# Kernel optimization log

Measured on AMD Instinct MI355X. Metric: run time of the kernel, lower is better.

Reference implementation:

```python
import jax, jax.numpy as jnp
import numpy as np

N_NODES = 100000
N_EDGES = 3200000
OUT_FEATURES = 16


def setup_inputs() -> dict:
    key = jax.random.key(0)
    k1, k2 = jax.random.split(key)
    edge = jax.random.randint(k1, (2, N_EDGES), 0, N_NODES, dtype=jnp.int64 if jax.config.jax_enable_x64 else jnp.int32)
    edge_w = jax.random.normal(k2, (N_EDGES, OUT_FEATURES), dtype=jnp.float32)
    return {
        "edge": edge,
        "edge_w": edge_w,
        "N": N_NODES,
        "E": N_EDGES,
        "out_features": OUT_FEATURES,
    }


def reference(edge, edge_w, N, E, out_features):
    # torch.sparse.sum over dim=1 of a [N, N, F] COO tensor == segment-sum of
    # edge_w grouped by the source index edge[0], producing dense [N, F].
    src = edge[0]  # [E]
    out = jax.ops.segment_sum(edge_w, src, num_segments=N)  # [N, F]
    return out
```

## Files before the change

kernel.cpp:

```cpp
#include <hip/hip_runtime.h>
#include <hip/hip_cooperative_groups.h>
#include <math.h>

namespace cg = cooperative_groups;


#define F 16
#define NPB 1024
#define NPB_SHIFT 10
#define MAXB 128
#define SCALE 256.0f
#define INV_SCALE (1.0f / 256.0f)

#define NBIN 256
#define BINT 512
#define NSPLIT 8
#define SLICES (NBIN / NSPLIT)
#define ACCT 512

#define FB 512
#define FT 512
#define NBIN2 512
#define NSPLIT2 8
#define SLICES2 (NBIN2 / NSPLIT2)

__device__ __forceinline__ unsigned long long qpack(float4 v) {
    long long q0 = (long long)__float2int_rn(v.x * SCALE);
    long long q1 = (long long)__float2int_rn(v.y * SCALE);
    long long q2 = (long long)__float2int_rn(v.z * SCALE);
    long long q3 = (long long)__float2int_rn(v.w * SCALE);
    return (unsigned long long)((q3 << 48) + (q2 << 32) + (q1 << 16) + q0);
}

__global__ __launch_bounds__(FT, 4) void spmm_fused(
    const int* __restrict__ src,
    const float* __restrict__ w,
    unsigned int* __restrict__ idbuf,
    unsigned int* __restrict__ cnt,
    unsigned long long* __restrict__ pbuf,
    float* __restrict__ out,
    int E, int B, int capb, int per_block, int N)
{
    __shared__ unsigned long long acc[NPB * 4];
    __shared__ unsigned int pos[MAXB];
    __shared__ unsigned int ksh[SLICES2];

    cg::grid_group grid = cg::this_grid();
    const int tid = threadIdx.x;
    const int bid = blockIdx.x;
    const int n4  = N * 4;
    unsigned long long* spill = pbuf + (size_t)NSPLIT2 * (size_t)n4;

    for (int i = tid; i < B; i += FT) pos[i] = 0;
    __syncthreads();

    const int lo = bid * per_block;
    const int hi = min(E, lo + per_block);
    for (int e = lo + tid * 2; e < hi; e += FT * 2) {
        int sa, sb = -1;
        if (e + 1 < hi) { int2 s2 = *(const int2*)(src + e); sa = s2.x; sb = s2.y; }
        else            { sa = src[e]; }
        {
            const int bk = sa >> NPB_SHIFT;
            const unsigned int off = (unsigned int)(sa & (NPB - 1));
            const unsigned int r = atomicAdd(&pos[bk], 1u);
            if (r < (unsigned int)capb) {
                idbuf[((size_t)bid * B + bk) * capb + r] = (off << 22) | (unsigned int)e;
            } else {
                const float4* wr = (const float4*)(w + (size_t)e * F);
                #pragma unroll
                for (int qq = 0; qq < 4; ++qq)
                    atomicAdd(&spill[(size_t)sa * 4 + qq], qpack(wr[qq]));
            }
        }
        if (sb >= 0) {
            const int e1 = e + 1;
            const int bk = sb >> NPB_SHIFT;
            const unsigned int off = (unsigned int)(sb & (NPB - 1));
            const unsigned int r = atomicAdd(&pos[bk], 1u);
            if (r < (unsigned int)capb) {
                idbuf[((size_t)bid * B + bk) * capb + r] = (off << 22) | (unsigned int)e1;
            } else {
                const float4* wr = (const float4*)(w + (size_t)e1 * F);
                #pragma unroll
                for (int qq = 0; qq < 4; ++qq)
                    atomicAdd(&spill[(size_t)sb * 4 + qq], qpack(wr[qq]));
            }
        }
    }
    __syncthreads();
    for (int i = tid; i < B; i += FT)
        cnt[bid * B + i] = min(pos[i], (unsigned int)capb);

    __threadfence();
    grid.sync();

    const int q    = tid & 3;
    const int ei   = tid >> 2;
    const int half = ei >> 6;
    const int e64  = ei & 63;

    for (int t = bid; t < B * NSPLIT2; t += FB) {
        const int b  = t >> 3;
        const int sp = t & 7;

        for (int i = tid; i < NPB * 4; i += FT) acc[i] = 0ULL;
        if (tid < SLICES2) ksh[tid] = cnt[(sp * SLICES2 + tid) * B + b];
        __syncthreads();

        for (int sl = 0; sl < SLICES2; sl += 16) {
            unsigned int ent[8];
            #pragma unroll
            for (int j = 0; j < 8; ++j) {
                const int s = sl + 2 * j + half;
                ent[j] = idbuf[((size_t)(sp * SLICES2 + s) * B + b) * capb + e64];
            }
            float4 vv[8];
            #pragma unroll
            for (int j = 0; j < 8; ++j) {
                unsigned int e = ent[j] & 0x3FFFFFu;
                e = min(e, (unsigned int)(E - 1));
                vv[j] = *(const float4*)(w + (size_t)e * F + q * 4);
            }
            #pragma unroll
            for (int j = 0; j < 8; ++j) {
                const int s = sl + 2 * j + half;
                if ((unsigned int)e64 < ksh[s]) {
                    const unsigned int off = ent[j] >> 22;
                    atomicAdd(&acc[off * 4 + q], qpack(vv[j]));
                }
            }
        }
        for (int s = half; s < SLICES2; s += 2) {
            const unsigned int k = ksh[s];
            for (unsigned int i = 64 + e64; i < k; i += 64) {
                const unsigned int entry =
                    idbuf[((size_t)(sp * SLICES2 + s) * B + b) * capb + i];
                const unsigned int off = entry >> 22;
                const unsigned int e   = entry & 0x3FFFFFu;
                const float4 v = *(const float4*)(w + (size_t)e * F + q * 4);
                atomicAdd(&acc[off * 4 + q], qpack(v));
            }
        }
        __syncthreads();

        const int nbase = b << NPB_SHIFT;
        const int lim = min(NPB, N - nbase);
        unsigned long long* dst = pbuf + (size_t)sp * n4 + (size_t)nbase * 4;
        for (int i = tid; i < lim * 4; i += FT) dst[i] = acc[i];
        __syncthreads();
    }

    __threadfence();
    grid.sync();

    for (int idx = bid * FT + tid; idx < n4; idx += FB * FT) {
        unsigned long long a = 0;
        #pragma unroll
        for (int s = 0; s < NSPLIT2 + 1; ++s) a += pbuf[(size_t)s * n4 + idx];
        long long tt = (long long)a;
        const int s0 = (int)(short)(tt & 0xffff);  tt = (tt - s0) >> 16;
        const int s1 = (int)(short)(tt & 0xffff);  tt = (tt - s1) >> 16;
        const int s2 = (int)(short)(tt & 0xffff);  tt = (tt - s2) >> 16;
        const int s3 = (int)(short)(tt & 0xffff);
        float4 o;
        o.x = (float)s0 * INV_SCALE;
        o.y = (float)s1 * INV_SCALE;
        o.z = (float)s2 * INV_SCALE;
        o.w = (float)s3 * INV_SCALE;
        ((float4*)out)[idx] = o;
    }
}

__global__ __launch_bounds__(BINT) void spmm_bin_id(
    const int* __restrict__ src,
    const float* __restrict__ w,
    unsigned int* __restrict__ idbuf,
    unsigned int* __restrict__ cnt,
    unsigned long long* __restrict__ spill,
    int E, int B, int capb, int per_block)
{
    __shared__ unsigned int pos[MAXB];
    const int tid = threadIdx.x;
    for (int i = tid; i < B; i += BINT) pos[i] = 0;
    __syncthreads();

    const int lo = blockIdx.x * per_block;
    const int hi = min(E, lo + per_block);

    for (int e = lo + tid; e < hi; e += BINT) {
        const int s = src[e];
        const int bk = s >> NPB_SHIFT;
        const unsigned int off = (unsigned int)(s & (NPB - 1));
        const unsigned int r = atomicAdd(&pos[bk], 1u);
        if (r < (unsigned int)capb) {
            idbuf[((size_t)blockIdx.x * B + bk) * capb + r] =
                (off << 22) | (unsigned int)e;
        } else {
            const float4* wr = (const float4*)(w + (size_t)e * F);
            #pragma unroll
            for (int q = 0; q < 4; ++q)
                atomicAdd(&spill[(size_t)s * 4 + q], qpack(wr[q]));
        }
    }
    __syncthreads();
    for (int i = tid; i < B; i += BINT)
        cnt[blockIdx.x * B + i] = min(pos[i], (unsigned int)capb);
}

__global__ __launch_bounds__(ACCT) void spmm_acc_g(
    const float* __restrict__ w,
    const unsigned int* __restrict__ idbuf,
    const unsigned int* __restrict__ cnt,
    unsigned long long* __restrict__ pbuf,
    int B, int capb, int N)
{
    __shared__ unsigned long long acc[NPB * 4];
    const int tid = threadIdx.x;
    const int b  = blockIdx.x >> 3;
    const int sp = blockIdx.x & 7;

    for (int i = tid; i < NPB * 4; i += ACCT) acc[i] = 0ULL;
    __syncthreads();

    const int q  = tid & 3;
    const int ei = tid >> 2;

    for (int sl = 0; sl < SLICES; ++sl) {
        const int blk = sp * SLICES + sl;
        const unsigned int k = cnt[blk * B + b];
        const unsigned int* base = idbuf + ((size_t)blk * B + b) * capb;
        for (unsigned int i = ei; i < k; i += ACCT / 4) {
            const unsigned int entry = base[i];
            const unsigned int off = entry >> 22;
            const unsigned int e   = entry & 0x3FFFFFu;
            const float4 v = *(const float4*)(w + (size_t)e * F + q * 4);
            atomicAdd(&acc[off * 4 + q], qpack(v));
        }
    }
    __syncthreads();

    const int nbase = b << NPB_SHIFT;
    const int lim = min(NPB, N - nbase);
    unsigned long long* dst = pbuf + (size_t)sp * ((size_t)N * 4) + (size_t)nbase * 4;
    for (int i = tid; i < lim * 4; i += ACCT) dst[i] = acc[i];
}

__global__ __launch_bounds__(256) void spmm_decode9(
    const unsigned long long* __restrict__ pbuf,
    float* __restrict__ out, int n4)
{
    const int idx = blockIdx.x * 256 + threadIdx.x;
    if (idx >= n4) return;
    unsigned long long a = 0;
    #pragma unroll
    for (int s = 0; s < NSPLIT + 1; ++s) a += pbuf[(size_t)s * n4 + idx];

    long long t = (long long)a;
    const int s0 = (int)(short)(t & 0xffff);  t = (t - s0) >> 16;
    const int s1 = (int)(short)(t & 0xffff);  t = (t - s1) >> 16;
    const int s2 = (int)(short)(t & 0xffff);  t = (t - s2) >> 16;
    const int s3 = (int)(short)(t & 0xffff);

    float4 o;
    o.x = (float)s0 * INV_SCALE;
    o.y = (float)s1 * INV_SCALE;
    o.z = (float)s2 * INV_SCALE;
    o.w = (float)s3 * INV_SCALE;
    ((float4*)out)[idx] = o;
}

__global__ __launch_bounds__(256) void spmm_scatter_gs(
    const int* __restrict__ src,
    const float* __restrict__ w,
    unsigned long long* __restrict__ ws,
    int total)
{
    const int stride = gridDim.x * blockDim.x;
    for (int idx = blockIdx.x * blockDim.x + threadIdx.x; idx < total; idx += stride) {
        const int e = idx >> 2, lane = idx & 3;
        const float4 v = ((const float4*)w)[idx];
        atomicAdd(&ws[src[e] * 4 + lane], qpack(v));
    }
}

__global__ __launch_bounds__(256) void spmm_decode1(
    const unsigned long long* __restrict__ ws,
    float* __restrict__ out, int n4)
{
    const int idx = blockIdx.x * 256 + threadIdx.x;
    if (idx >= n4) return;
    long long t = (long long)ws[idx];
    const int s0 = (int)(short)(t & 0xffff);  t = (t - s0) >> 16;
    const int s1 = (int)(short)(t & 0xffff);  t = (t - s1) >> 16;
    const int s2 = (int)(short)(t & 0xffff);  t = (t - s2) >> 16;
    const int s3 = (int)(short)(t & 0xffff);
    float4 o;
    o.x = (float)s0 * INV_SCALE;
    o.y = (float)s1 * INV_SCALE;
    o.z = (float)s2 * INV_SCALE;
    o.w = (float)s3 * INV_SCALE;
    ((float4*)out)[idx] = o;
}

extern "C" void kernel_launch(void* const* d_in, const int* in_sizes, int n_in,
                              void* d_out, int out_size, void* d_ws, size_t ws_size,
                              hipStream_t stream) {
    const int* edge = (const int*)d_in[0];
    const float* ew = (const float*)d_in[1];
    const int E = in_sizes[0] / 2;
    const int N = out_size / F;
    const int n4 = N * 4;
    float* out = (float*)d_out;

    const int B = (N + NPB - 1) >> NPB_SHIFT;

    static int coop_state = -1;
    if (coop_state < 0) {
        int maxb = 0, cus = 0;
        hipDeviceProp_t prop;
        int dev = 0;
        hipError_t e1 = hipGetDevice(&dev);
        hipError_t e2 = hipGetDeviceProperties(&prop, dev);
        if (e2 == hipSuccess) cus = prop.multiProcessorCount;
        hipError_t e3 = hipOccupancyMaxActiveBlocksPerMultiprocessor(
            &maxb, spmm_fused, FT, 0);
        coop_state = (e1 == hipSuccess && e3 == hipSuccess &&
                      (long)maxb * (long)cus >= FB) ? 1 : 0;
    }

    const double mean2 = (double)E / ((double)NBIN2 * (double)B);
    int capb2 = (int)(mean2 + 8.0 * sqrt(mean2 > 1.0 ? mean2 : 1.0) + 16.0);
    capb2 = (capb2 + 15) & ~15;
    const size_t idbuf2_b = (size_t)NBIN2 * B * capb2 * 4;
    size_t off_cnt2  = (idbuf2_b + 255) & ~(size_t)255;
    const size_t cnt2_b = (size_t)NBIN2 * B * 4;
    size_t off_pbuf2 = (off_cnt2 + cnt2_b + 255) & ~(size_t)255;
    const size_t pbuf2_b = (size_t)(NSPLIT2 + 1) * n4 * 8;
    const size_t need2 = off_pbuf2 + pbuf2_b;

    const double mean = (double)E / ((double)NBIN * (double)B);
    int capb = (int)(mean + 8.0 * sqrt(mean > 1.0 ? mean : 1.0) + 16.0);
    capb = (capb + 15) & ~15;
    const size_t idbuf_b = (size_t)NBIN * B * capb * 4;
    size_t off_cnt  = (idbuf_b + 255) & ~(size_t)255;
    const size_t cnt_b = (size_t)NBIN * B * 4;
    size_t off_pbuf = (off_cnt + cnt_b + 255) & ~(size_t)255;
    const size_t pbuf_b = (size_t)(NSPLIT + 1) * n4 * 8;
    const size_t need = off_pbuf + pbuf_b;

    const int block = 256;
    const bool shape_ok = (B <= MAXB) && (E > 0) && (E < (1 << 22));

    if (shape_ok && coop_state == 1 && need2 <= ws_size) {
        unsigned int* idbuf = (unsigned int*)d_ws;
        unsigned int* cnt   = (unsigned int*)((char*)d_ws + off_cnt2);
        unsigned long long* pbuf = (unsigned long long*)((char*)d_ws + off_pbuf2);
        unsigned long long* spill = pbuf + (size_t)NSPLIT2 * n4;

        hipMemsetAsync(spill, 0, (size_t)n4 * 8, stream);

        int per_block2 = (E + FB - 1) / FB;
        per_block2 = (per_block2 + 1) & ~1;

        int E_ = E, B_ = B, N_ = N, cap_ = capb2, pb_ = per_block2;
        void* kargs[] = { (void*)&edge, (void*)&ew, (void*)&idbuf, (void*)&cnt,
                          (void*)&pbuf, (void*)&out,
                          (void*)&E_, (void*)&B_, (void*)&cap_, (void*)&pb_, (void*)&N_ };
        hipError_t lr = hipLaunchCooperativeKernel(
            spmm_fused, dim3(FB), dim3(FT), kargs, 0, stream);
        if (lr == hipSuccess) return;
        coop_state = 0;
    }

    if (shape_ok && need <= ws_size) {
        unsigned int* idbuf = (unsigned int*)d_ws;
        unsigned int* cnt   = (unsigned int*)((char*)d_ws + off_cnt);
        unsigned long long* pbuf  = (unsigned long long*)((char*)d_ws + off_pbuf);
        unsigned long long* spill = pbuf + (size_t)NSPLIT * n4;

        hipMemsetAsync(spill, 0, (size_t)n4 * 8, stream);

        const int per_block = (E + NBIN - 1) / NBIN;
        spmm_bin_id<<<NBIN, BINT, 0, stream>>>(edge, ew, idbuf, cnt, spill,
                                               E, B, capb, per_block);
        spmm_acc_g<<<B * NSPLIT, ACCT, 0, stream>>>(ew, idbuf, cnt, pbuf,
                                                    B, capb, N);
        spmm_decode9<<<(n4 + block - 1) / block, block, 0, stream>>>(pbuf, out, n4);
    } else {
        unsigned long long* ws = (unsigned long long*)d_ws;
        hipMemsetAsync(ws, 0, (size_t)n4 * 8, stream);
        spmm_scatter_gs<<<2048, block, 0, stream>>>(edge, ew, ws, E * 4);
        spmm_decode1<<<(n4 + block - 1) / block, block, 0, stream>>>(ws, out, n4);
    }
}
```

Measured before the change: 355.6 us.

## Double cooperative grid and bin count, remap slice-gather threads, fit capacity to workspace

Doubles the cooperative grid to 1024 blocks and the per-block source bins to 1024, raising the launch-bounds occupancy hint to 8 blocks. The gather phase is reorganised so 16 lanes per slice walk up to 64 entries with a count guard. This replaces the unconditional clamped loads of the old code. Entries past 64 are now handled by a single thread per slice in a serial loop. Bucket capacity uses a tighter margin and is capped to the available workspace, with a minimum-capacity check before the fused path is chosen. More blocks and bins aim to spread the binning and accumulation work across more of the device, at the cost of smaller per-bin lists, a serial overflow tail and a larger count array.

```diff
diff --git a/kernel.cpp b/kernel.cpp
--- a/kernel.cpp
+++ b/kernel.cpp
@@ -18,9 +18,9 @@
 #define SLICES (NBIN / NSPLIT)
 #define ACCT 512
 
-#define FB 512
+#define FB 1024
 #define FT 512
-#define NBIN2 512
+#define NBIN2 1024
 #define NSPLIT2 8
 #define SLICES2 (NBIN2 / NSPLIT2)
 
@@ -32,7 +32,7 @@
     return (unsigned long long)((q3 << 48) + (q2 << 32) + (q1 << 16) + q0);
 }
 
-__global__ __launch_bounds__(FT, 4) void spmm_fused(
+__global__ __launch_bounds__(FT, 8) void spmm_fused(
     const int* __restrict__ src,
     const float* __restrict__ w,
     unsigned int* __restrict__ idbuf,
@@ -95,10 +95,10 @@
     __threadfence();
     grid.sync();
 
-    const int q    = tid & 3;
-    const int ei   = tid >> 2;
-    const int half = ei >> 6;
-    const int e64  = ei & 63;
+    const int q   = tid & 3;
+    const int st  = tid >> 2;
+    const int sg  = st >> 4;
+    const int s16 = st & 15;
 
     for (int t = bid; t < B * NSPLIT2; t += FB) {
         const int b  = t >> 3;
@@ -108,38 +108,36 @@
         if (tid < SLICES2) ksh[tid] = cnt[(sp * SLICES2 + tid) * B + b];
         __syncthreads();
 
-        for (int sl = 0; sl < SLICES2; sl += 16) {
-            unsigned int ent[8];
+        for (int sr = 0; sr < 16; ++sr) {
+            const int s   = sr * 8 + sg;
+            const int blk = sp * SLICES2 + s;
+            const unsigned int k = ksh[s];
+            const unsigned int* cell = idbuf + ((size_t)blk * B + b) * capb;
             #pragma unroll
-            for (int j = 0; j < 8; ++j) {
-                const int s = sl + 2 * j + half;
-                ent[j] = idbuf[((size_t)(sp * SLICES2 + s) * B + b) * capb + e64];
-            }
-            float4 vv[8];
-            #pragma unroll
-            for (int j = 0; j < 8; ++j) {
-                unsigned int e = ent[j] & 0x3FFFFFu;
-                e = min(e, (unsigned int)(E - 1));
-                vv[j] = *(const float4*)(w + (size_t)e * F + q * 4);
-            }
-            #pragma unroll
-            for (int j = 0; j < 8; ++j) {
-                const int s = sl + 2 * j + half;
-                if ((unsigned int)e64 < ksh[s]) {
-                    const unsigned int off = ent[j] >> 22;
-                    atomicAdd(&acc[off * 4 + q], qpack(vv[j]));
+            for (int tr = 0; tr < 4; ++tr) {
+                const unsigned int slot = (unsigned int)(tr * 16 + s16);
+                if (slot < k) {
+                    const unsigned int entry = cell[slot];
+                    const unsigned int off = entry >> 22;
+                    const unsigned int e   = entry & 0x3FFFFFu;
+                    const float4 v = *(const float4*)(w + (size_t)e * F + q * 4);
+                    atomicAdd(&acc[off * 4 + q], qpack(v));
                 }
             }
         }
-        for (int s = half; s < SLICES2; s += 2) {
+        {
+            const int s = st;
             const unsigned int k = ksh[s];
-            for (unsigned int i = 64 + e64; i < k; i += 64) {
-                const unsigned int entry =
-                    idbuf[((size_t)(sp * SLICES2 + s) * B + b) * capb + i];
-                const unsigned int off = entry >> 22;
-                const unsigned int e   = entry & 0x3FFFFFu;
-                const float4 v = *(const float4*)(w + (size_t)e * F + q * 4);
-                atomicAdd(&acc[off * 4 + q], qpack(v));
+            if (k > 64u) {
+                const int blk = sp * SLICES2 + s;
+                const unsigned int* cell = idbuf + ((size_t)blk * B + b) * capb;
+                for (unsigned int i = 64u; i < k; ++i) {
+                    const unsigned int entry = cell[i];
+                    const unsigned int off = entry >> 22;
+                    const unsigned int e   = entry & 0x3FFFFFu;
+                    const float4 v = *(const float4*)(w + (size_t)e * F + q * 4);
+                    atomicAdd(&acc[off * 4 + q], qpack(v));
+                }
             }
         }
         __syncthreads();
@@ -330,13 +328,22 @@
     }
 
     const double mean2 = (double)E / ((double)NBIN2 * (double)B);
-    int capb2 = (int)(mean2 + 8.0 * sqrt(mean2 > 1.0 ? mean2 : 1.0) + 16.0);
+    const double sig2  = sqrt(mean2 > 1.0 ? mean2 : 1.0);
+    int capb2 = (int)(mean2 + 6.0 * sig2 + 8.0);
     capb2 = (capb2 + 15) & ~15;
+    const size_t cnt2_b  = (size_t)NBIN2 * B * 4;
+    const size_t pbuf2_b = (size_t)(NSPLIT2 + 1) * n4 * 8;
+    const size_t fixed2  = ((cnt2_b + 255) & ~(size_t)255) + pbuf2_b + 512;
+    if (ws_size > fixed2) {
+        const size_t idroom = ws_size - fixed2;
+        int capb2_max = (int)(idroom / ((size_t)NBIN2 * B * 4));
+        capb2_max &= ~15;
+        if (capb2 > capb2_max) capb2 = capb2_max;
+    }
+    const int capb2_min = ((int)(mean2 + 3.0 * sig2) + 15) & ~15;
     const size_t idbuf2_b = (size_t)NBIN2 * B * capb2 * 4;
     size_t off_cnt2  = (idbuf2_b + 255) & ~(size_t)255;
-    const size_t cnt2_b = (size_t)NBIN2 * B * 4;
     size_t off_pbuf2 = (off_cnt2 + cnt2_b + 255) & ~(size_t)255;
-    const size_t pbuf2_b = (size_t)(NSPLIT2 + 1) * n4 * 8;
     const size_t need2 = off_pbuf2 + pbuf2_b;
 
     const double mean = (double)E / ((double)NBIN * (double)B);
@@ -352,7 +359,8 @@
     const int block = 256;
     const bool shape_ok = (B <= MAXB) && (E > 0) && (E < (1 << 22));
 
-    if (shape_ok && coop_state == 1 && need2 <= ws_size) {
+    if (shape_ok && coop_state == 1 && capb2 >= capb2_min && capb2 >= 16 &&
+        need2 <= ws_size) {
         unsigned int* idbuf = (unsigned int*)d_ws;
         unsigned int* cnt   = (unsigned int*)((char*)d_ws + off_cnt2);
         unsigned long long* pbuf = (unsigned long long*)((char*)d_ws + off_pbuf2);
```

Result: no change. 355.2 us (-0.1%).
